# Performance work log

Measured on AMD Instinct MI355X. Metric: run time of the kernel, lower is better.

Reference implementation:

```python
import jax, jax.numpy as jnp
import numpy as np

H = 256  # hidden_size
B = 8192  # batch
S = 1024  # seq_length


def setup_inputs() -> dict:
    key = jax.random.key(0)
    ks = jax.random.split(key, 12)
    lim_g = 1.0 / np.sqrt(1 + H)  # torch Linear default init bound, fan_in = 1+H
    lim_o = 1.0 / np.sqrt(H)
    def lin(k, out_dim, in_dim, lim):
        kw, kb = jax.random.split(k)
        W = jax.random.uniform(kw, (out_dim, in_dim), jnp.float32, -lim, lim)
        b = jax.random.uniform(kb, (out_dim,), jnp.float32, -lim, lim)
        return W, b
    Wf, bf = lin(ks[0], H, 1 + H, lim_g)
    Wi, bi = lin(ks[1], H, 1 + H, lim_g)
    Wc, bc = lin(ks[2], H, 1 + H, lim_g)
    Wo, bo = lin(ks[3], H, 1 + H, lim_g)
    Wout, bout = lin(ks[4], 1, H, lim_o)
    x = jax.random.normal(ks[5], (B, S), jnp.float32)
    return {"x": x, "Wf": Wf, "bf": bf, "Wi": Wi, "bi": bi,
            "Wc": Wc, "bc": bc, "Wo": Wo, "bo": bo,
            "Wout": Wout, "bout": bout}


def reference(x, Wf, bf, Wi, bi, Wc, bc, Wo, bo, Wout, bout):
    B_, S_ = x.shape
    H_ = Wf.shape[0]
    # Fuse the four gate linears into one GEMM per step (same math):
    Wall = jnp.concatenate([Wf, Wi, Wc, Wo], axis=0)      # [4H, 1+H]
    ball = jnp.concatenate([bf, bi, bc, bo], axis=0)      # [4H]

    def step(carry, xt):
        h, c = carry                                       # [B,H], [B,H]
        conc = jnp.concatenate([xt[:, None], h], axis=1)   # [B, 1+H]
        g = conc @ Wall.T + ball                           # [B, 4H]
        f, i, cs, o = jnp.split(g, 4, axis=1)
        c = jax.nn.sigmoid(f) * c + jax.nn.sigmoid(i) * jnp.tanh(cs)
        h = jax.nn.sigmoid(o) * jnp.tanh(c)
        return (h, c), None

    h0 = jnp.zeros((B_, H_), x.dtype)
    c0 = jnp.zeros((B_, H_), x.dtype)
    (h, _), _ = jax.lax.scan(step, (h0, c0), x.T)          # scan over seq axis
    out = h @ Wout.T + bout                                # [B, 1]
    return out.squeeze(-1)                                 # [B]
```

## Files before the change

### kernel.cpp

```cpp
#include <hip/hip_runtime.h>
#include <hip/hip_fp16.h>


typedef _Float16 f16x8 __attribute__((ext_vector_type(8)));
typedef float f32x4 __attribute__((ext_vector_type(4)));
typedef unsigned int u32;
typedef unsigned short u16;

#define WINT_OFF 0u
#define W0B_OFF  524288u
#define FLAG_OFF 528384u
#define PUB_OFF  1048576u

static __device__ __forceinline__ float fast_exp2(float x) {
#if __has_builtin(__builtin_amdgcn_exp2f)
  return __builtin_amdgcn_exp2f(x);
#else
  return exp2f(x);
#endif
}
static __device__ __forceinline__ float fast_rcp(float x) {
#if __has_builtin(__builtin_amdgcn_rcpf)
  return __builtin_amdgcn_rcpf(x);
#else
  return 1.0f / x;
#endif
}
static __device__ __forceinline__ float fsig(float x) {
  return fast_rcp(1.0f + fast_exp2(-1.44269504f * x));
}
static __device__ __forceinline__ float ftanh_(float x) {
  float e = fast_exp2(2.88539008f * x);
  return 1.0f - 2.0f * fast_rcp(e + 1.0f);
}
static __device__ __forceinline__ u16 f16b(float f) {
  union { _Float16 h; u16 u; } cv; cv.h = (_Float16)f; return cv.u;
}
static __device__ __forceinline__ float h2f(u16 u) {
  union { u16 u; _Float16 h; } cv; cv.u = u; return (float)cv.h;
}
static __device__ __forceinline__ u16* pub_base(u16* pub, int set, int par,
                                                int pid, int half) {
  return pub + ((size_t)(((set * 2 + par) * 128 + pid) * 2 + half) << 12);
}

__global__ void lstm_prep(const float* __restrict__ Wf, const float* __restrict__ Wi,
                          const float* __restrict__ Wc, const float* __restrict__ Wo,
                          const float* __restrict__ bf_, const float* __restrict__ bi_,
                          const float* __restrict__ bc_, const float* __restrict__ bo_,
                          u16* __restrict__ Wint, u32* __restrict__ w0b) {
  int n = blockIdx.x;
  int k = threadIdx.x;
  int g = n >> 8, j = n & 255;
  const float* Ws = (g == 0) ? Wf : (g == 1) ? Wi : (g == 2) ? Wc : Wo;
  Wint[n * 256 + k] = f16b(Ws[j * 257 + 1 + k]);
  if (k == 0) {
    const float* bs = (g == 0) ? bf_ : (g == 1) ? bi_ : (g == 2) ? bc_ : bo_;
    w0b[n] = (u32)f16b(Ws[j * 257]) | ((u32)f16b(bs[j]) << 16);
  }
}

__global__ void lstm_zero(uint4* __restrict__ pub4, uint4* __restrict__ flags4,
                          float* __restrict__ out, const float* __restrict__ bout) {
  int idx = blockIdx.x * 256 + threadIdx.x;
  uint4 z = uint4{0, 0, 0, 0};
  if (idx < 131072) pub4[idx] = z;
  else if (idx < 262144) pub4[idx + 131072] = z;
  else if (idx < 264192) flags4[idx - 262144] = z;
  else { int o = idx - 264192; if (o < 8192) out[o] = bout[0]; }
}

__global__ __launch_bounds__(512, 2) void lstm_main(
    const u16* __restrict__ Wint, const u32* __restrict__ w0b,
    const float* __restrict__ x, const float* __restrict__ Wout,
    float* __restrict__ out, u16* __restrict__ pub, int* __restrict__ flags) {

  __shared__ __align__(16) u16 stg[2][2][4096];

  const int tid  = threadIdx.x;
  const int wv   = tid >> 6;
  const int lane = tid & 63;
  const int l15  = lane & 15;
  const int quad = lane >> 4;
  const int B    = blockIdx.x;
  const int mi   = (B >> 3) & 1;
  const int peer = B ^ 8;
  const int pid  = (B & 7) | ((B >> 4) << 3);
  const int rows0 = pid * 64;

  f16x8 wfrag[4][8];
#pragma unroll
  for (int g = 0; g < 4; ++g)
#pragma unroll
    for (int hm = 0; hm < 2; ++hm)
#pragma unroll
      for (int ktl = 0; ktl < 4; ++ktl) {
        int kbase = (hm == 0 ? mi : 1 - mi) * 128 + ktl * 32;
        wfrag[g][hm * 4 + ktl] = *(const f16x8*)(Wint +
            (size_t)(g * 256 + mi * 128 + wv * 16 + l15) * 256 + kbase + quad * 8);
      }
  uint4 w0bv[4];
#pragma unroll
  for (int g = 0; g < 4; ++g)
    w0bv[g] = *(const uint4*)(w0b + g * 256 + mi * 128 + wv * 16 + quad * 4);

#pragma unroll
  for (int i = 0; i < 4; ++i) ((uint4*)stg)[tid + i * 512] = uint4{0, 0, 0, 0};

  float cst[2][2][4];
#pragma unroll
  for (int s = 0; s < 2; ++s)
#pragma unroll
    for (int bt = 0; bt < 2; ++bt)
#pragma unroll
      for (int r = 0; r < 4; ++r) cst[s][bt][r] = 0.0f;

  const float* xq = x + (size_t)rows0 * 1024;
  float xcur[2][2];
#pragma unroll
  for (int s = 0; s < 2; ++s)
#pragma unroll
    for (int bt = 0; bt < 2; ++bt)
      xcur[s][bt] = xq[(size_t)(s * 32 + bt * 16 + l15) * 1024];

  int* const myflag = flags + B * 32;
  int* const pfl    = flags + peer * 32;

  __syncthreads();

#pragma unroll 1
  for (int t = 0; t < 1024; ++t) {
#pragma unroll
    for (int s = 0; s < 2; ++s) {
      f32x4 acc[4][2];
#pragma unroll
      for (int g = 0; g < 4; ++g) {
        u32 pka[4] = {w0bv[g].x, w0bv[g].y, w0bv[g].z, w0bv[g].w};
#pragma unroll
        for (int r = 0; r < 4; ++r) {
          float w0f = h2f((u16)pka[r]), bsf = h2f((u16)(pka[r] >> 16));
          acc[g][0][r] = xcur[s][0] * w0f + bsf;
          acc[g][1][r] = xcur[s][1] * w0f + bsf;
        }
      }
#pragma unroll
      for (int bt = 0; bt < 2; ++bt)
        xcur[s][bt] = xq[(size_t)(s * 32 + bt * 16 + l15) * 1024 + ((t + 1) & 1023)];

#pragma unroll
      for (int hm = 0; hm < 2; ++hm)
#pragma unroll
        for (int ktl = 0; ktl < 4; ++ktl) {
          f16x8 bb[2];
#pragma unroll
          for (int bt = 0; bt < 2; ++bt) {
            int b = bt * 16 + l15;
            int cp = (ktl * 4 + quad) ^ (b & 15);
            bb[bt] = *(const f16x8*)(&stg[s][hm][0] + b * 128 + cp * 8);
          }
#pragma unroll
          for (int g = 0; g < 4; ++g)
#pragma unroll
            for (int bt = 0; bt < 2; ++bt)
              acc[g][bt] = __builtin_amdgcn_mfma_f32_16x16x32_f16(
                  wfrag[g][hm * 4 + ktl], bb[bt], acc[g][bt], 0, 0, 0);
        }

      const int tn = (s == 0) ? t : t + 1;
      if (tn < 1024) {
        while (__hip_atomic_load(pfl + (s ^ 1) * 16, __ATOMIC_RELAXED,
                                 __HIP_MEMORY_SCOPE_AGENT) < tn)
          __builtin_amdgcn_s_sleep(1);
        const u16* srcO = pub_base(pub, s ^ 1, tn & 1, pid, mi);
        const u16* srcP = pub_base(pub, s ^ 1, tn & 1, pid, 1 - mi);
        __builtin_amdgcn_global_load_lds(
            (const __attribute__((address_space(1))) u32*)(srcO + wv * 512 + lane * 8),
            (__attribute__((address_space(3))) u32*)(&stg[s ^ 1][0][wv * 512]), 16, 0, 0);
        __builtin_amdgcn_global_load_lds(
            (const __attribute__((address_space(1))) u32*)(srcP + wv * 512 + lane * 8),
            (__attribute__((address_space(3))) u32*)(&stg[s ^ 1][1][wv * 512]), 16, 0, 0);
      }

      u16* pb = pub_base(pub, s, (t + 1) & 1, pid, mi);
#pragma unroll
      for (int bt = 0; bt < 2; ++bt) {
        int b = bt * 16 + l15;
        u32 lo, hi;
        {
          float h0, h1, h2, h3;
#pragma unroll
          for (int r = 0; r < 4; ++r) {
            float fg = acc[0][bt][r], ig = acc[1][bt][r];
            float cg = acc[2][bt][r], og = acc[3][bt][r];
            float c_ = fsig(fg) * cst[s][bt][r] + fsig(ig) * ftanh_(cg);
            cst[s][bt][r] = c_;
            float hv = fsig(og) * ftanh_(c_);
            if (r == 0) h0 = hv; else if (r == 1) h1 = hv;
            else if (r == 2) h2 = hv; else h3 = hv;
          }
          lo = (u32)f16b(h0) | ((u32)f16b(h1) << 16);
          hi = (u32)f16b(h2) | ((u32)f16b(h3) << 16);
        }
        int c16 = wv * 2 + (quad >> 1);
        int cp  = c16 ^ (b & 15);
        *(uint2*)(pb + b * 128 + cp * 8 + (quad & 1) * 4) = uint2{lo, hi};
      }

      __syncthreads();
      if (tid == 0)
        __hip_atomic_store(myflag + s * 16, t + 1, __ATOMIC_RELAXED,
                           __HIP_MEMORY_SCOPE_AGENT);
    }
  }

  if (tid < 64) {
    int s = tid >> 5, b = tid & 31;
    const u16* pbase = pub_base(pub, s, 0, pid, mi);
    float a = 0.0f;
#pragma unroll
    for (int c = 0; c < 16; ++c) {
      f16x8 hv = *(const f16x8*)(pbase + b * 128 + ((c ^ (b & 15)) * 8));
#pragma unroll
      for (int e = 0; e < 8; ++e) a += (float)hv[e] * Wout[mi * 128 + c * 8 + e];
    }
    atomicAdd(&out[rows0 + s * 32 + b], a);
  }
}

extern "C" void kernel_launch(void* const* d_in, const int* in_sizes, int n_in,
                              void* d_out, int out_size, void* d_ws, size_t ws_size,
                              hipStream_t stream) {
  const float* x    = (const float*)d_in[0];
  const float* Wf   = (const float*)d_in[1];
  const float* bf_  = (const float*)d_in[2];
  const float* Wi   = (const float*)d_in[3];
  const float* bi_  = (const float*)d_in[4];
  const float* Wc   = (const float*)d_in[5];
  const float* bc_  = (const float*)d_in[6];
  const float* Wo   = (const float*)d_in[7];
  const float* bo_  = (const float*)d_in[8];
  const float* Wout = (const float*)d_in[9];
  const float* bout = (const float*)d_in[10];

  u16* Wint  = (u16*)((char*)d_ws + WINT_OFF);
  u32* w0b   = (u32*)((char*)d_ws + W0B_OFF);
  int* flags = (int*)((char*)d_ws + FLAG_OFF);
  u16* pub   = (u16*)((char*)d_ws + PUB_OFF);

  lstm_prep<<<1024, 256, 0, stream>>>(Wf, Wi, Wc, Wo, bf_, bi_, bc_, bo_, Wint, w0b);
  lstm_zero<<<1064, 256, 0, stream>>>((uint4*)pub, (uint4*)flags, (float*)d_out, bout);
  lstm_main<<<256, 512, 0, stream>>>(Wint, w0b, x, Wout, (float*)d_out, pub, flags);
}
```

Baseline: 4.925 ms.

## Fold activation scales into weights, interleave gate MFMAs with exp, write own h to LDS

The log2(e) and 2·log2(e) factors are folded into the fp16 gate weights and biases during prep, so sigmoid and tanh become a bare exp2 followed by one combined rational expression with fewer reciprocals. The MFMA chains are reordered per batch tile and gate so the exp2 work for finished gates overlaps the remaining MFMAs. Each block now writes its own half of h straight into a double-buffered LDS stage, so it only fetches the peer's half from global memory. This doubles LDS usage, and the scaled fp16 weights plus the merged formula (with c clamped to ±40) may slightly change numerical precision.

```diff
diff --git a/kernel.cpp b/kernel.cpp
--- a/kernel.cpp
+++ b/kernel.cpp
@@ -25,13 +25,6 @@
 #else
   return 1.0f / x;
 #endif
-}
-static __device__ __forceinline__ float fsig(float x) {
-  return fast_rcp(1.0f + fast_exp2(-1.44269504f * x));
-}
-static __device__ __forceinline__ float ftanh_(float x) {
-  float e = fast_exp2(2.88539008f * x);
-  return 1.0f - 2.0f * fast_rcp(e + 1.0f);
 }
 static __device__ __forceinline__ u16 f16b(float f) {
   union { _Float16 h; u16 u; } cv; cv.h = (_Float16)f; return cv.u;
@@ -53,10 +46,11 @@
   int k = threadIdx.x;
   int g = n >> 8, j = n & 255;
   const float* Ws = (g == 0) ? Wf : (g == 1) ? Wi : (g == 2) ? Wc : Wo;
-  Wint[n * 256 + k] = f16b(Ws[j * 257 + 1 + k]);
+  const float scale = (g == 2) ? 2.88539008f : 1.44269504f;
+  Wint[n * 256 + k] = f16b(Ws[j * 257 + 1 + k] * scale);
   if (k == 0) {
     const float* bs = (g == 0) ? bf_ : (g == 1) ? bi_ : (g == 2) ? bc_ : bo_;
-    w0b[n] = (u32)f16b(Ws[j * 257]) | ((u32)f16b(bs[j]) << 16);
+    w0b[n] = (u32)f16b(Ws[j * 257] * scale) | ((u32)f16b(bs[j] * scale) << 16);
   }
 }
 
@@ -75,7 +69,7 @@
     const float* __restrict__ x, const float* __restrict__ Wout,
     float* __restrict__ out, u16* __restrict__ pub, int* __restrict__ flags) {
 
-  __shared__ __align__(16) u16 stg[2][2][4096];
+  __shared__ __align__(16) u16 stg[2][2][2][4096];
 
   const int tid  = threadIdx.x;
   const int wv   = tid >> 6;
@@ -105,7 +99,7 @@
     w0bv[g] = *(const uint4*)(w0b + g * 256 + mi * 128 + wv * 16 + quad * 4);
 
 #pragma unroll
-  for (int i = 0; i < 4; ++i) ((uint4*)stg)[tid + i * 512] = uint4{0, 0, 0, 0};
+  for (int i = 0; i < 8; ++i) ((uint4*)stg)[tid + i * 512] = uint4{0, 0, 0, 0};
 
   float cst[2][2][4];
 #pragma unroll
@@ -127,6 +121,55 @@
   int* const pfl    = flags + peer * 32;
 
   __syncthreads();
+
+#define GCHAIN(G, BT) do {                                                     \
+    _Pragma("unroll")                                                          \
+    for (int sl_ = 0; sl_ < 8; ++sl_)                                          \
+      acc[G][BT] = __builtin_amdgcn_mfma_f32_16x16x32_f16(                     \
+          wfrag[G][sl_], bb[sl_], acc[G][BT], 0, 0, 0);                        \
+  } while (0)
+
+#define FRONT(G, BT, SGN) do {                                                 \
+    _Pragma("unroll")                                                          \
+    for (int r_ = 0; r_ < 4; ++r_)                                             \
+      acc[G][BT][r_] = fast_exp2((SGN) * acc[G][BT][r_]);                      \
+  } while (0)
+
+#define LOADBB(S, PAR, BT) do {                                                \
+    int b_ = (BT) * 16 + l15;                                                  \
+    _Pragma("unroll")                                                          \
+    for (int sl_ = 0; sl_ < 8; ++sl_) {                                        \
+      int cp_ = ((sl_ & 3) * 4 + quad) ^ (b_ & 15);                            \
+      bb[sl_] = *(const f16x8*)(&stg[S][PAR][sl_ >> 2][0] + b_ * 128 + cp_ * 8); \
+    }                                                                          \
+  } while (0)
+
+#define COMBINE_PUB(S, BT) do {                                                \
+    int b_ = (BT) * 16 + l15;                                                  \
+    float h0_, h1_, h2_, h3_;                                                  \
+    _Pragma("unroll")                                                          \
+    for (int r_ = 0; r_ < 4; ++r_) {                                           \
+      float Ef_ = acc[0][BT][r_], Ei_ = acc[1][BT][r_];                        \
+      float C_  = acc[2][BT][r_];                                              \
+      float Eo_ = fast_exp2(-acc[3][BT][r_]);                                  \
+      float X_  = 1.0f + Ef_;                                                  \
+      float Y_  = (1.0f + Ei_) * (C_ + 1.0f);                                  \
+      float num_ = cst[S][BT][r_] * Y_ + (C_ - 1.0f) * X_;                     \
+      float c2_  = num_ * fast_rcp(X_ * Y_);                                   \
+      cst[S][BT][r_] = c2_;                                                    \
+      float cc_ = fminf(fmaxf(c2_, -40.0f), 40.0f);                            \
+      float T_  = fast_exp2(2.88539008f * cc_);                                \
+      float hv_ = (T_ - 1.0f) * fast_rcp((1.0f + Eo_) * (T_ + 1.0f));          \
+      if (r_ == 0) h0_ = hv_; else if (r_ == 1) h1_ = hv_;                     \
+      else if (r_ == 2) h2_ = hv_; else h3_ = hv_;                             \
+    }                                                                          \
+    u32 lo_ = (u32)f16b(h0_) | ((u32)f16b(h1_) << 16);                         \
+    u32 hi_ = (u32)f16b(h2_) | ((u32)f16b(h3_) << 16);                         \
+    int c16_ = wv * 2 + (quad >> 1);                                           \
+    int off_ = b_ * 128 + (c16_ ^ (b_ & 15)) * 8 + (quad & 1) * 4;             \
+    *(uint2*)(lb + off_) = uint2{lo_, hi_};                                    \
+    *(uint2*)(pb + off_) = uint2{lo_, hi_};                                    \
+  } while (0)
 
 #pragma unroll 1
   for (int t = 0; t < 1024; ++t) {
@@ -147,64 +190,36 @@
       for (int bt = 0; bt < 2; ++bt)
         xcur[s][bt] = xq[(size_t)(s * 32 + bt * 16 + l15) * 1024 + ((t + 1) & 1023)];
 
-#pragma unroll
-      for (int hm = 0; hm < 2; ++hm)
-#pragma unroll
-        for (int ktl = 0; ktl < 4; ++ktl) {
-          f16x8 bb[2];
-#pragma unroll
-          for (int bt = 0; bt < 2; ++bt) {
-            int b = bt * 16 + l15;
-            int cp = (ktl * 4 + quad) ^ (b & 15);
-            bb[bt] = *(const f16x8*)(&stg[s][hm][0] + b * 128 + cp * 8);
-          }
-#pragma unroll
-          for (int g = 0; g < 4; ++g)
-#pragma unroll
-            for (int bt = 0; bt < 2; ++bt)
-              acc[g][bt] = __builtin_amdgcn_mfma_f32_16x16x32_f16(
-                  wfrag[g][hm * 4 + ktl], bb[bt], acc[g][bt], 0, 0, 0);
-        }
+      u16* pb = pub_base(pub, s, (t + 1) & 1, pid, mi);
+      u16* lb = &stg[s][(t + 1) & 1][0][0];
+      f16x8 bb[8];
+
+      LOADBB(s, t & 1, 0);
+      GCHAIN(0, 0);
+      GCHAIN(1, 0); FRONT(0, 0, -1.0f);
+      GCHAIN(2, 0); FRONT(1, 0, -1.0f);
+      GCHAIN(3, 0); FRONT(2, 0,  1.0f);
+      COMBINE_PUB(s, 0);
+
+      LOADBB(s, t & 1, 1);
+      GCHAIN(0, 1);
+      GCHAIN(1, 1); FRONT(0, 1, -1.0f);
+      GCHAIN(2, 1); FRONT(1, 1, -1.0f);
+      GCHAIN(3, 1); FRONT(2, 1,  1.0f);
 
       const int tn = (s == 0) ? t : t + 1;
       if (tn < 1024) {
         while (__hip_atomic_load(pfl + (s ^ 1) * 16, __ATOMIC_RELAXED,
                                  __HIP_MEMORY_SCOPE_AGENT) < tn)
           __builtin_amdgcn_s_sleep(1);
-        const u16* srcO = pub_base(pub, s ^ 1, tn & 1, pid, mi);
         const u16* srcP = pub_base(pub, s ^ 1, tn & 1, pid, 1 - mi);
         __builtin_amdgcn_global_load_lds(
-            (const __attribute__((address_space(1))) u32*)(srcO + wv * 512 + lane * 8),
-            (__attribute__((address_space(3))) u32*)(&stg[s ^ 1][0][wv * 512]), 16, 0, 0);
-        __builtin_amdgcn_global_load_lds(
             (const __attribute__((address_space(1))) u32*)(srcP + wv * 512 + lane * 8),
-            (__attribute__((address_space(3))) u32*)(&stg[s ^ 1][1][wv * 512]), 16, 0, 0);
+            (__attribute__((address_space(3))) u32*)(&stg[s ^ 1][tn & 1][1][wv * 512]),
+            16, 0, 0);
       }
 
-      u16* pb = pub_base(pub, s, (t + 1) & 1, pid, mi);
-#pragma unroll
-      for (int bt = 0; bt < 2; ++bt) {
-        int b = bt * 16 + l15;
-        u32 lo, hi;
-        {
-          float h0, h1, h2, h3;
-#pragma unroll
-          for (int r = 0; r < 4; ++r) {
-            float fg = acc[0][bt][r], ig = acc[1][bt][r];
-            float cg = acc[2][bt][r], og = acc[3][bt][r];
-            float c_ = fsig(fg) * cst[s][bt][r] + fsig(ig) * ftanh_(cg);
-            cst[s][bt][r] = c_;
-            float hv = fsig(og) * ftanh_(c_);
-            if (r == 0) h0 = hv; else if (r == 1) h1 = hv;
-            else if (r == 2) h2 = hv; else h3 = hv;
-          }
-          lo = (u32)f16b(h0) | ((u32)f16b(h1) << 16);
-          hi = (u32)f16b(h2) | ((u32)f16b(h3) << 16);
-        }
-        int c16 = wv * 2 + (quad >> 1);
-        int cp  = c16 ^ (b & 15);
-        *(uint2*)(pb + b * 128 + cp * 8 + (quad & 1) * 4) = uint2{lo, hi};
-      }
+      COMBINE_PUB(s, 1);
 
       __syncthreads();
       if (tid == 0)
@@ -225,6 +240,10 @@
     }
     atomicAdd(&out[rows0 + s * 32 + b], a);
   }
+#undef GCHAIN
+#undef FRONT
+#undef LOADBB
+#undef COMBINE_PUB
 }
 
 extern "C" void kernel_launch(void* const* d_in, const int* in_sizes, int n_in,
```

After: 4.957 ms. About the same (+0.6%).
